# Optimization experiments

Measured on AMD Instinct MI355X. Metric: run time of the kernel, lower is better.

The kernel has to match this reference:

```python
import jax, jax.numpy as jnp
import numpy as np

NUM_HEADS = 16

def setup_inputs() -> dict:
    key = jax.random.key(0)
    ks = jax.random.split(key, 12)
    S, B, E = 128, 16, 1024
    N, H, L = NUM_HEADS, 1024 // NUM_HEADS, 2048
    w = 0.02  # weight init scale
    return {
        "query": jax.random.normal(ks[0], (S, B, E), jnp.float32),
        "key": jax.random.normal(ks[1], (S, B, E), jnp.float32),
        "k_cache": jax.random.normal(ks[2], (B, N, L, H), jnp.float32),
        "v_cache": jax.random.normal(ks[3], (B, N, L, H), jnp.float32),
        "Wq": jax.random.normal(ks[4], (E, E), jnp.float32) * w,
        "bq": jax.random.normal(ks[5], (E,), jnp.float32) * w,
        "Wk": jax.random.normal(ks[6], (E, E), jnp.float32) * w,
        "bk": jax.random.normal(ks[7], (E,), jnp.float32) * w,
        "Wv": jax.random.normal(ks[8], (E, E), jnp.float32) * w,
        "bv": jax.random.normal(ks[9], (E,), jnp.float32) * w,
        "Wo": jax.random.normal(ks[10], (E, E), jnp.float32) * w,
        "bo": jax.random.normal(ks[11], (E,), jnp.float32) * w,
    }


def reference(query, key, k_cache, v_cache, Wq, bq, Wk, bk, Wv, bv, Wo, bo):
    # Decoder self-attention with KV cache (use_past=True path).
    S, B, E = query.shape
    N = NUM_HEADS
    H = E // N
    scaling = H ** -0.5

    # q/k/v projections (torch Linear: x @ W.T + b)
    q = (query @ Wq.T + bq) * scaling            # [S, B, E]
    k_new = query @ Wk.T + bk                    # [S, B, E]
    v_new = query @ Wv.T + bv

    # reshape to [B*N, S, H]
    def shape(x):
        return jnp.transpose(x.reshape(S, B * N, H), (1, 0, 2))

    q = shape(q)
    k_new = shape(k_new)
    v_new = shape(v_new)

    # concat KV cache along time: cache [B,N,L,H] -> [B*N,L,H]
    L = k_cache.shape[2]
    k = jnp.concatenate([k_cache.reshape(B * N, L, H), k_new], axis=1)  # [B*N, L+S, H]
    v = jnp.concatenate([v_cache.reshape(B * N, L, H), v_new], axis=1)

    attn = jax.nn.softmax(jnp.einsum('bth,bsh->bts', q, k), axis=-1)    # [B*N, S, L+S]
    out = jnp.einsum('bts,bsh->bth', attn, v)                           # [B*N, S, H]
    out = jnp.transpose(out, (1, 0, 2)).reshape(S, B, E)
    out = out @ Wo.T + bo

    new_key_cache = k.reshape(B, N, L + S, H)
    new_value_cache = v.reshape(B, N, L + S, H)
    return out, new_key_cache, new_value_cache
```

## Files before the change

### kernel.cpp

```cpp
#include <hip/hip_runtime.h>

#define S_Q     128
#define B_B     16
#define E_E     1024
#define N_H     16
#define H_D     64
#define L_C     2048
#define T_T     2176
#define BN_H    256
#define M_M     2048
#define KC_OFF  2097152
#define VC_OFF  37748736

typedef __attribute__((ext_vector_type(8))) short short8v;
typedef __attribute__((ext_vector_type(4))) short short4v;
typedef __attribute__((ext_vector_type(4))) float floatx4;

__device__ __forceinline__ short f2bf(float f) {
  union { float f; unsigned u; } x; x.f = f;
  unsigned r = x.u + 0x7fffu + ((x.u >> 16) & 1u);
  return (short)(r >> 16);
}
__device__ __forceinline__ short4v f2bf4(float4 v) {
  short4v r; r.x = f2bf(v.x); r.y = f2bf(v.y); r.z = f2bf(v.z); r.w = f2bf(v.w);
  return r;
}

__global__ __launch_bounds__(256) void copy_caches(const float4* __restrict__ ksrc,
                                                   const float4* __restrict__ vsrc,
                                                   float* __restrict__ out) {
  float4* __restrict__ kdst = (float4*)(out + KC_OFF);
  float4* __restrict__ vdst = (float4*)(out + VC_OFF);
  const int TH4 = T_T * H_D / 4;
  const long total = (long)BN_H * (L_C * H_D / 4);
  const long stride = (long)gridDim.x * blockDim.x;
#pragma unroll 1
  for (long i = (long)blockIdx.x * blockDim.x + threadIdx.x; i < total; i += stride) {
    long bn  = i >> 15;
    long rem = i & 32767;
    long d   = bn * TH4 + rem;
    kdst[d] = ksrc[i];
    vdst[d] = vsrc[i];
  }
}

__global__ __launch_bounds__(256) void gemm64(
    const float* __restrict__ X,
    const float* __restrict__ W0, const float* __restrict__ Bi0,
    const float* __restrict__ W1, const float* __restrict__ Bi1,
    const float* __restrict__ W2, const float* __restrict__ Bi2,
    short* __restrict__ qws, float* __restrict__ obase, int mode)
{
  __shared__ short lA[64 * 64];
  __shared__ short lB[64 * 64];
  const int z   = blockIdx.z;
  const float* W  = (z == 0) ? W0 : (z == 1) ? W1 : W2;
  const float* Bi = (z == 0) ? Bi0 : (z == 1) ? Bi1 : Bi2;
  const int gr0 = blockIdx.x * 64;
  const int gc0 = blockIdx.y * 64;
  const int tid = threadIdx.x;
  const int lane = tid & 63;
  const int wid  = tid >> 6;
  const int wm = (wid & 1) * 32;
  const int wn = (wid >> 1) * 32;
  const int c = lane & 15;
  const int g = lane >> 4;

  floatx4 zero4 = {0.f, 0.f, 0.f, 0.f};
  floatx4 acc[2][2];
  acc[0][0] = zero4; acc[0][1] = zero4; acc[1][0] = zero4; acc[1][1] = zero4;

  int srow[4], scol[4];
  float4 ra[4], rb[4];
#pragma unroll
  for (int j = 0; j < 4; ++j) { int idx = tid + j * 256; srow[j] = idx >> 4; scol[j] = (idx & 15) * 4; }

  auto stage_load = [&](int kt) {
#pragma unroll
    for (int j = 0; j < 4; ++j) {
      ra[j] = *(const float4*)&X[(long)(gr0 + srow[j]) * 1024 + kt * 64 + scol[j]];
      rb[j] = *(const float4*)&W[(long)(gc0 + srow[j]) * 1024 + kt * 64 + scol[j]];
    }
  };
  stage_load(0);

  for (int kt = 0; kt < 16; ++kt) {
    __syncthreads();
#pragma unroll
    for (int j = 0; j < 4; ++j) {
      int sidx = (srow[j] * 64 + scol[j]) ^ ((srow[j] & 7) << 3);
      *(short4v*)&lA[sidx] = f2bf4(ra[j]);
      *(short4v*)&lB[sidx] = f2bf4(rb[j]);
    }
    __syncthreads();
    if (kt < 15) stage_load(kt + 1);
#pragma unroll
    for (int ks = 0; ks < 2; ++ks) {
      short8v af[2], bf[2];
#pragma unroll
      for (int mi = 0; mi < 2; ++mi) {
        int row = wm + mi * 16 + c;
        af[mi] = *(const short8v*)&lA[(row * 64 + ks * 32 + g * 8) ^ ((c & 7) << 3)];
      }
#pragma unroll
      for (int ni = 0; ni < 2; ++ni) {
        int row = wn + ni * 16 + c;
        bf[ni] = *(const short8v*)&lB[(row * 64 + ks * 32 + g * 8) ^ ((c & 7) << 3)];
      }
#pragma unroll
      for (int mi = 0; mi < 2; ++mi)
#pragma unroll
        for (int ni = 0; ni < 2; ++ni)
          acc[mi][ni] = __builtin_amdgcn_mfma_f32_16x16x32_bf16(af[mi], bf[ni], acc[mi][ni], 0, 0, 0);
    }
  }

#pragma unroll
  for (int mi = 0; mi < 2; ++mi) {
#pragma unroll
    for (int ni = 0; ni < 2; ++ni) {
#pragma unroll
      for (int r = 0; r < 4; ++r) {
        int m = gr0 + wm + mi * 16 + g * 4 + r;
        int n = gc0 + wn + ni * 16 + c;
        float v = acc[mi][ni][r] + Bi[n];
        if (mode == 1) {
          obase[(long)m * 1024 + n] = v;
        } else {
          int s = m >> 4, b = m & 15, nh = n >> 6, h = n & 63;
          if (z == 0) {
            qws[(((long)(b * 16 + nh) * 128 + s) << 6) + h] = f2bf(v * 0.125f);
          } else {
            long off = (z == 1) ? (long)KC_OFF : (long)VC_OFF;
            obase[off + (((long)(b * 16 + nh) * T_T + L_C + s) << 6) + h] = v;
          }
        }
      }
    }
  }
}

__global__ __launch_bounds__(512) void attn_kernel(const short* __restrict__ qws,
                                                   const float* __restrict__ dout,
                                                   float* __restrict__ ctx)
{
  __shared__ short lK[64 * 64];
  __shared__ short lV[64 * 72];
  __shared__ short lP[8 * 16 * 72];

  const int bn = blockIdx.x;
  const int tid = threadIdx.x;
  const int lane = tid & 63;
  const int wid  = tid >> 6;
  const int c = lane & 15;
  const int g = lane >> 4;
  const float* kcache = dout + KC_OFF + (long)bn * (T_T * H_D);
  const float* vcache = dout + VC_OFF + (long)bn * (T_T * H_D);

  short8v aq[2];
#pragma unroll
  for (int ks = 0; ks < 2; ++ks)
    aq[ks] = *(const short8v*)&qws[(((long)bn * 128 + wid * 16 + c) << 6) + ks * 32 + g * 8];

  floatx4 zero4 = {0.f, 0.f, 0.f, 0.f};
  floatx4 o[4];
#pragma unroll
  for (int nb = 0; nb < 4; ++nb) o[nb] = zero4;
  float mr[4], lr[4];
#pragma unroll
  for (int r = 0; r < 4; ++r) { mr[r] = -1e30f; lr[r] = 0.f; }

  int srow[2], scol[2];
  float4 rk[2], rv[2];
#pragma unroll
  for (int j = 0; j < 2; ++j) { int idx = tid + j * 512; srow[j] = idx >> 4; scol[j] = (idx & 15) * 4; }

  auto load_tile = [&](int t) {
#pragma unroll
    for (int j = 0; j < 2; ++j) {
      long base = (((long)(t * 64 + srow[j])) << 6) + scol[j];
      rk[j] = *(const float4*)&kcache[base];
      rv[j] = *(const float4*)&vcache[base];
    }
  };
  load_tile(0);

  short* lPw = lP + wid * (16 * 72);
  const int NT = T_T / 64;

  for (int t = 0; t < NT; ++t) {
    __syncthreads();
#pragma unroll
    for (int j = 0; j < 2; ++j) {
      int sidx = (srow[j] * 64 + scol[j]) ^ ((srow[j] & 7) << 3);
      *(short4v*)&lK[sidx] = f2bf4(rk[j]);
      const float* pv = (const float*)&rv[j];
#pragma unroll
      for (int e = 0; e < 4; ++e)
        lV[(scol[j] + e) * 72 + srow[j]] = f2bf(pv[e]);
    }
    __syncthreads();
    if (t + 1 < NT) load_tile(t + 1);

    floatx4 sc[4];
#pragma unroll
    for (int kb = 0; kb < 4; ++kb) {
      sc[kb] = zero4;
#pragma unroll
      for (int ks = 0; ks < 2; ++ks) {
        int row = kb * 16 + c;
        short8v kf = *(const short8v*)&lK[(row * 64 + ks * 32 + g * 8) ^ ((c & 7) << 3)];
        sc[kb] = __builtin_amdgcn_mfma_f32_16x16x32_bf16(aq[ks], kf, sc[kb], 0, 0, 0);
      }
    }

    float corr[4];
#pragma unroll
    for (int r = 0; r < 4; ++r) {
      float mt = fmaxf(fmaxf(sc[0][r], sc[1][r]), fmaxf(sc[2][r], sc[3][r]));
#pragma unroll
      for (int msk = 1; msk < 16; msk <<= 1)
        mt = fmaxf(mt, __shfl_xor(mt, msk, 64));
      float mnew = fmaxf(mr[r], mt);
      float co = __expf(mr[r] - mnew);
      float ps = 0.f;
#pragma unroll
      for (int kb = 0; kb < 4; ++kb) {
        float p = __expf(sc[kb][r] - mnew);
        sc[kb][r] = p;
        ps += p;
      }
#pragma unroll
      for (int msk = 1; msk < 16; msk <<= 1)
        ps += __shfl_xor(ps, msk, 64);
      lr[r] = lr[r] * co + ps;
      mr[r] = mnew;
      corr[r] = co;
    }
#pragma unroll
    for (int nb = 0; nb < 4; ++nb)
#pragma unroll
      for (int r = 0; r < 4; ++r)
        o[nb][r] *= corr[r];

#pragma unroll
    for (int kb = 0; kb < 4; ++kb)
#pragma unroll
      for (int r = 0; r < 4; ++r)
        lPw[(g * 4 + r) * 72 + kb * 16 + c] = f2bf(sc[kb][r]);
    asm volatile("s_waitcnt lgkmcnt(0)" ::: "memory");

#pragma unroll
    for (int ks = 0; ks < 2; ++ks) {
      short8v ap = *(const short8v*)&lPw[c * 72 + ks * 32 + g * 8];
#pragma unroll
      for (int nb = 0; nb < 4; ++nb) {
        short8v vf = *(const short8v*)&lV[(nb * 16 + c) * 72 + ks * 32 + g * 8];
        o[nb] = __builtin_amdgcn_mfma_f32_16x16x32_bf16(ap, vf, o[nb], 0, 0, 0);
      }
    }
  }

  const int b = bn >> 4, nh = bn & 15;
#pragma unroll
  for (int r = 0; r < 4; ++r) {
    float inv = 1.0f / lr[r];
    int s = wid * 16 + g * 4 + r;
#pragma unroll
    for (int nb = 0; nb < 4; ++nb)
      ctx[(long)(s * 16 + b) * 1024 + nh * 64 + nb * 16 + c] = o[nb][r] * inv;
  }
}

extern "C" void kernel_launch(void* const* d_in, const int* in_sizes, int n_in,
                              void* d_out, int out_size, void* d_ws, size_t ws_size,
                              hipStream_t stream) {
  const float* query = (const float*)d_in[0];
  const float* kc = (const float*)d_in[2];
  const float* vc = (const float*)d_in[3];
  const float* Wq = (const float*)d_in[4];
  const float* bq = (const float*)d_in[5];
  const float* Wk = (const float*)d_in[6];
  const float* bk = (const float*)d_in[7];
  const float* Wv = (const float*)d_in[8];
  const float* bv = (const float*)d_in[9];
  const float* Wo = (const float*)d_in[10];
  const float* bo = (const float*)d_in[11];

  float* out = (float*)d_out;
  float* ctx = (float*)d_ws;
  short* qws = (short*)((char*)d_ws + (size_t)8 * 1024 * 1024);

  copy_caches<<<dim3(2048), dim3(256), 0, stream>>>((const float4*)kc, (const float4*)vc, out);
  gemm64<<<dim3(32, 16, 3), dim3(256), 0, stream>>>(query, Wq, bq, Wk, bk, Wv, bv, qws, out, 0);
  attn_kernel<<<dim3(256), dim3(512), 0, stream>>>(qws, out, ctx);
  gemm64<<<dim3(32, 16, 1), dim3(256), 0, stream>>>(ctx, Wo, bo, Wo, bo, Wo, bo, qws, out, 1);
}
```

Before: 646.8 us.

## Fuse KV cache copy into attention kernel and raise MFMA wave priority

Removes the separate cache-copy kernel. The attention kernel now reads the original K/V caches directly and writes them into the output cache region while it streams them, so the caches are read once instead of being written and then read back. It also moves the next-tile prefetch before the barrier and wraps the MFMA sections in s_setprio to favour matrix work. The new stores add write traffic inside the attention loop, and only 256 blocks carry the full copy bandwidth.

```diff
diff --git a/kernel.cpp b/kernel.cpp
--- a/kernel.cpp
+++ b/kernel.cpp
@@ -24,24 +24,6 @@
 __device__ __forceinline__ short4v f2bf4(float4 v) {
   short4v r; r.x = f2bf(v.x); r.y = f2bf(v.y); r.z = f2bf(v.z); r.w = f2bf(v.w);
   return r;
-}
-
-__global__ __launch_bounds__(256) void copy_caches(const float4* __restrict__ ksrc,
-                                                   const float4* __restrict__ vsrc,
-                                                   float* __restrict__ out) {
-  float4* __restrict__ kdst = (float4*)(out + KC_OFF);
-  float4* __restrict__ vdst = (float4*)(out + VC_OFF);
-  const int TH4 = T_T * H_D / 4;
-  const long total = (long)BN_H * (L_C * H_D / 4);
-  const long stride = (long)gridDim.x * blockDim.x;
-#pragma unroll 1
-  for (long i = (long)blockIdx.x * blockDim.x + threadIdx.x; i < total; i += stride) {
-    long bn  = i >> 15;
-    long rem = i & 32767;
-    long d   = bn * TH4 + rem;
-    kdst[d] = ksrc[i];
-    vdst[d] = vsrc[i];
-  }
 }
 
 __global__ __launch_bounds__(256) void gemm64(
@@ -140,9 +122,11 @@
   }
 }
 
-__global__ __launch_bounds__(512) void attn_kernel(const short* __restrict__ qws,
-                                                   const float* __restrict__ dout,
-                                                   float* __restrict__ ctx)
+__global__ __launch_bounds__(512) void attn_fused(const short* __restrict__ qws,
+                                                  const float* __restrict__ kc_in,
+                                                  const float* __restrict__ vc_in,
+                                                  float* __restrict__ dout,
+                                                  float* __restrict__ ctx)
 {
   __shared__ short lK[64 * 64];
   __shared__ short lV[64 * 72];
@@ -154,8 +138,11 @@
   const int wid  = tid >> 6;
   const int c = lane & 15;
   const int g = lane >> 4;
-  const float* kcache = dout + KC_OFF + (long)bn * (T_T * H_D);
-  const float* vcache = dout + VC_OFF + (long)bn * (T_T * H_D);
+
+  const float* ksrc = kc_in + (long)bn * (L_C * H_D);
+  const float* vsrc = vc_in + (long)bn * (L_C * H_D);
+  float* kdst = dout + KC_OFF + (long)bn * (T_T * H_D);
+  float* vdst = dout + VC_OFF + (long)bn * (T_T * H_D);
 
   short8v aq[2];
 #pragma unroll
@@ -175,18 +162,27 @@
 #pragma unroll
   for (int j = 0; j < 2; ++j) { int idx = tid + j * 512; srow[j] = idx >> 4; scol[j] = (idx & 15) * 4; }
 
+  const int NT = T_T / 64;
   auto load_tile = [&](int t) {
-#pragma unroll
-    for (int j = 0; j < 2; ++j) {
-      long base = (((long)(t * 64 + srow[j])) << 6) + scol[j];
-      rk[j] = *(const float4*)&kcache[base];
-      rv[j] = *(const float4*)&vcache[base];
+    if (t < 32) {
+#pragma unroll
+      for (int j = 0; j < 2; ++j) {
+        long base = (((long)(t * 64 + srow[j])) << 6) + scol[j];
+        rk[j] = *(const float4*)&ksrc[base];
+        rv[j] = *(const float4*)&vsrc[base];
+      }
+    } else {
+#pragma unroll
+      for (int j = 0; j < 2; ++j) {
+        long base = (((long)(t * 64 + srow[j])) << 6) + scol[j];
+        rk[j] = *(const float4*)&kdst[base];
+        rv[j] = *(const float4*)&vdst[base];
+      }
     }
   };
   load_tile(0);
 
   short* lPw = lP + wid * (16 * 72);
-  const int NT = T_T / 64;
 
   for (int t = 0; t < NT; ++t) {
     __syncthreads();
@@ -199,10 +195,19 @@
       for (int e = 0; e < 4; ++e)
         lV[(scol[j] + e) * 72 + srow[j]] = f2bf(pv[e]);
     }
+    if (t < 32) {
+#pragma unroll
+      for (int j = 0; j < 2; ++j) {
+        long base = (((long)(t * 64 + srow[j])) << 6) + scol[j];
+        *(float4*)&kdst[base] = rk[j];
+        *(float4*)&vdst[base] = rv[j];
+      }
+    }
+    if (t + 1 < NT) load_tile(t + 1);
     __syncthreads();
-    if (t + 1 < NT) load_tile(t + 1);
 
     floatx4 sc[4];
+    __builtin_amdgcn_s_setprio(1);
 #pragma unroll
     for (int kb = 0; kb < 4; ++kb) {
       sc[kb] = zero4;
@@ -213,6 +218,7 @@
         sc[kb] = __builtin_amdgcn_mfma_f32_16x16x32_bf16(aq[ks], kf, sc[kb], 0, 0, 0);
       }
     }
+    __builtin_amdgcn_s_setprio(0);
 
     float corr[4];
 #pragma unroll
@@ -250,6 +256,7 @@
         lPw[(g * 4 + r) * 72 + kb * 16 + c] = f2bf(sc[kb][r]);
     asm volatile("s_waitcnt lgkmcnt(0)" ::: "memory");
 
+    __builtin_amdgcn_s_setprio(1);
 #pragma unroll
     for (int ks = 0; ks < 2; ++ks) {
       short8v ap = *(const short8v*)&lPw[c * 72 + ks * 32 + g * 8];
@@ -259,6 +266,7 @@
         o[nb] = __builtin_amdgcn_mfma_f32_16x16x32_bf16(ap, vf, o[nb], 0, 0, 0);
       }
     }
+    __builtin_amdgcn_s_setprio(0);
   }
 
   const int b = bn >> 4, nh = bn & 15;
@@ -291,8 +299,7 @@
   float* ctx = (float*)d_ws;
   short* qws = (short*)((char*)d_ws + (size_t)8 * 1024 * 1024);
 
-  copy_caches<<<dim3(2048), dim3(256), 0, stream>>>((const float4*)kc, (const float4*)vc, out);
   gemm64<<<dim3(32, 16, 3), dim3(256), 0, stream>>>(query, Wq, bq, Wk, bk, Wv, bv, qws, out, 0);
-  attn_kernel<<<dim3(256), dim3(512), 0, stream>>>(qws, out, ctx);
+  attn_fused<<<dim3(256), dim3(512), 0, stream>>>(qws, kc, vc, out, ctx);
   gemm64<<<dim3(32, 16, 1), dim3(256), 0, stream>>>(ctx, Wo, bo, Wo, bo, Wo, bo, qws, out, 1);
 }
```

Result: faster. 581.3 us (-10.1%).
